# Performance work log

Hardware: AMD Instinct MI355X
Metric: run time of the kernel (lower is better)

## Reference

```python
import jax, jax.numpy as jnp
import numpy as np


def _local_indices(H, W, K):
    # KxK local window per pixel; border neighbors clamped to the image (replicate padding)
    half = K // 2
    d = np.arange(-half, half + 1)
    r = np.clip(np.arange(H)[:, None, None, None] + d[None, None, :, None], 0, H - 1)
    c = np.clip(np.arange(W)[None, :, None, None] + d[None, None, None, :], 0, W - 1)
    return (r * W + c).reshape(H * W, K * K).astype(np.int32)


def setup_inputs():
    B, C, H, W = 2, 32, 128, 128
    K, S = 25, 1024
    N = H * W
    k1, k2, k3, k4 = jax.random.split(jax.random.key(0), 4)
    key_feat = jax.random.normal(k1, (B, C, H, W), dtype=jnp.float32)
    query_feat = jax.random.normal(k2, (B, C, H, W), dtype=jnp.float32)
    segment_target = jax.random.randint(k3, (B, 1, H, W), 0, 64, dtype=jnp.int32)
    local = jnp.broadcast_to(jnp.asarray(_local_indices(H, W, K))[None], (B, N, K * K))
    rand_glob = jax.random.randint(k4, (B, N, S - K * K), 0, N, dtype=jnp.int32)
    sample_inds = jnp.concatenate([local, rand_glob], axis=-1)  # [B, N, S]
    return {"key_feat": key_feat, "query_feat": query_feat,
            "segment_target": segment_target, "sample_inds": sample_inds}


def _affinity_logits(key_f, query_f, sample_inds, chunk=1024):
    # key_f, query_f: [B, N, C]; sample_inds: [B, N, S]
    B, N, C = key_f.shape
    S = sample_inds.shape[-1]
    nchunks = N // chunk
    q_c = query_f.reshape(B, nchunks, chunk, C).transpose(1, 0, 2, 3)
    i_c = sample_inds.reshape(B, nchunks, chunk, S).transpose(1, 0, 2, 3)

    def body(carry, args):
        q, idx = args                                   # [B, chunk, C], [B, chunk, S]
        kg = jax.vmap(lambda kb, ib: kb[ib])(key_f, idx)  # [B, chunk, S, C]
        return carry, jnp.einsum('bnsc,bnc->bns', kg, q)

    _, lc = jax.lax.scan(body, None, (q_c, i_c))        # [nchunks, B, chunk, S]
    logits = lc.transpose(1, 0, 2, 3).reshape(B, N, S)
    return logits * (C ** -0.5)


def _loss(logits, sample_inds, segment_target):
    B, N, S = logits.shape
    seg = segment_target.reshape(B, N)
    samples = jax.vmap(lambda s, i: s[i])(seg, sample_inds)      # [B, N, S]
    targets = (seg[:, :, None] == samples).astype(logits.dtype)
    mask = (seg != 0).astype(logits.dtype)[:, :, None]           # [B, N, 1]
    # weighted_softmax(logits, mask)
    xe = jnp.exp(logits - jnp.max(logits, -1, keepdims=True))
    denom = jnp.sum(xe * mask, -1, keepdims=True)
    y_prob = xe * mask / (denom + 1e-9)
    y_pred = jnp.log(jnp.clip(y_prob, 1e-8, None))
    y_true = targets / (jnp.sum(targets, -1, keepdims=True) + 1e-9)
    # F.kl_div(y_pred, y_true, reduction='none') with 0*log(0) = 0
    kl = jnp.where(y_true > 0,
                   y_true * (jnp.log(jnp.clip(y_true, 1e-30, None)) - y_pred),
                   0.0) * mask
    agg_mask = (jnp.sum(mask, -1) > 0).astype(logits.dtype)
    return jnp.sum(kl) / (jnp.sum(agg_mask) + 1e-9)


def reference(key_feat, query_feat, segment_target, sample_inds):
    B, C, H, W = key_feat.shape
    N = H * W
    key_f = key_feat.reshape(B, C, N).transpose(0, 2, 1)    # [B, N, C]
    query_f = query_feat.reshape(B, C, N).transpose(0, 2, 1)
    logits = _affinity_logits(key_f, query_f, sample_inds)  # [B, N, S], scaled by C**-0.5
    loss = _loss(logits, sample_inds, segment_target)
    return (logits, loss)
```

## Files before the change

### kernel.cpp

```cpp
#include <hip/hip_runtime.h>
#include <stdint.h>

typedef _Float16 h2 __attribute__((ext_vector_type(2)));

static constexpr int CDIM = 32;
static constexpr int NPIX = 16384;
static constexpr int SSAM = 1024;

__device__ __forceinline__ uint16_t f2h(float f) {
    union { _Float16 h; uint16_t u; } c;
    c.h = (_Float16)f;
    return c.u;
}

template<int CTRL>
__device__ __forceinline__ float dpp_add(float x) {
    int y = __builtin_amdgcn_mov_dpp(__float_as_int(x), CTRL, 0xF, 0xF, true);
    return x + __int_as_float(y);
}

__device__ __forceinline__ float dot2(h2 a, h2 b, float c) {
    return __builtin_amdgcn_fdot2(a, b, c, false);
}

__global__ __launch_bounds__(256)
void prep_kernel(const float* __restrict__ key_f,
                 const float* __restrict__ query_f,
                 const int* __restrict__ seg32,
                 uint8_t* __restrict__ key16,
                 uint8_t* __restrict__ q16,
                 uint8_t* __restrict__ seg8,
                 int N, int rows, float scale)
{
    int gI = blockIdx.x * 256 + threadIdx.x;
    if (gI >= rows) return;
    int b = gI / N, n = gI - b * N;
    const size_t cb = (size_t)b * CDIM;

    uint32_t kp[16], qp[16];
#pragma unroll
    for (int c = 0; c < CDIM; c += 2) {
        float k0 = key_f[(cb + c) * N + n];
        float k1 = key_f[(cb + c + 1) * N + n];
        float q0 = query_f[(cb + c) * N + n] * scale;
        float q1 = query_f[(cb + c + 1) * N + n] * scale;
        kp[c >> 1] = (uint32_t)f2h(k0) | ((uint32_t)f2h(k1) << 16);
        qp[c >> 1] = (uint32_t)f2h(q0) | ((uint32_t)f2h(q1) << 16);
    }
    uint4* ko = (uint4*)(key16 + ((size_t)gI << 6));
    uint4* qo = (uint4*)(q16 + ((size_t)gI << 6));
#pragma unroll
    for (int j = 0; j < 4; ++j) {
        ko[j] = make_uint4(kp[4*j], kp[4*j+1], kp[4*j+2], kp[4*j+3]);
        qo[j] = make_uint4(qp[4*j], qp[4*j+1], qp[4*j+2], qp[4*j+3]);
    }
    seg8[gI] = (uint8_t)seg32[gI];
}

__global__ __launch_bounds__(256)
void affinity_coop(const int* __restrict__ inds,
                   const uint8_t* __restrict__ key16,
                   const uint8_t* __restrict__ q16,
                   const uint8_t* __restrict__ seg8,
                   float* __restrict__ out,
                   float* __restrict__ ws_kl)
{
    const int bid  = blockIdx.x;
    const int tid  = threadIdx.x;
    const int b    = bid >> 14;
    const int lane = tid & 63;
    const int w    = tid >> 6;
    const int g    = lane >> 2;
    const int sub  = lane & 3;

    __shared__ __align__(16) int     idx_lds[SSAM];
    __shared__ __align__(16) uint8_t seg_lds[NPIX];
    __shared__ float redA[4], redB[4], redC[4];

    const size_t rowbase = (size_t)bid * SSAM;

    ((int4*)idx_lds)[tid] = ((const int4*)(inds + rowbase))[tid];

    const uint8_t* sbg = seg8 + ((size_t)b << 14);
#pragma unroll
    for (int r = 0; r < 4; ++r)
        ((uint4*)seg_lds)[(r << 8) + tid] = ((const uint4*)sbg)[(r << 8) + tid];

    h2 qh[4];
    {
        union { uint4 u; h2 h[4]; } qc;
        qc.u = *(const uint4*)(q16 + ((size_t)bid << 6) + (sub << 4));
        qh[0] = qc.h[0]; qh[1] = qc.h[1]; qh[2] = qc.h[2]; qh[3] = qc.h[3];
    }
    __syncthreads();

    const int seg_n = (int)seg_lds[bid & 0x3FFF];
    const uint8_t* kb = key16 + ((size_t)b << 20);
    const uint32_t subs = (uint32_t)(sub << 4);
    const int sbase = (w << 8) + g;

    int idxs[16];
#pragma unroll
    for (int i = 0; i < 16; ++i)
        idxs[i] = idx_lds[sbase + (i << 4)];

    uint4 kd[16];
#pragma unroll
    for (int i = 0; i < 16; ++i)
        kd[i] = *(const uint4*)(kb + (((uint32_t)idxs[i] << 6) | subs));

    float lgo[4];
    float m = -1e30f;
#pragma unroll
    for (int i = 0; i < 16; ++i) {
        union { uint4 u; h2 h[4]; } kc; kc.u = kd[i];
        float acc = dot2(kc.h[0], qh[0], 0.f);
        acc = dot2(kc.h[1], qh[1], acc);
        acc = dot2(kc.h[2], qh[2], acc);
        acc = dot2(kc.h[3], qh[3], acc);
        acc = dpp_add<0xB1>(acc);
        acc = dpp_add<0x4E>(acc);
        m = fmaxf(m, acc);
        if (sub == (i & 3)) lgo[i >> 2] = acc;
        if (sub == 0) out[rowbase + sbase + (i << 4)] = acc;
    }

    int tfm = 0;
#pragma unroll
    for (int j = 0; j < 4; ++j) {
        int idx = idx_lds[sbase + ((((j << 2) | sub)) << 4)];
        if ((int)seg_lds[idx] == seg_n) tfm |= 1 << j;
    }

#pragma unroll
    for (int off = 32; off >= 4; off >>= 1)
        m = fmaxf(m, __shfl_xor(m, off, 64));
    if (lane == 0) redA[w] = m;
    __syncthreads();
    m = fmaxf(fmaxf(redA[0], redA[1]), fmaxf(redA[2], redA[3]));

    float e[4];
    float z = 0.f, tcnt = (float)__popc((unsigned)tfm);
#pragma unroll
    for (int j = 0; j < 4; ++j) {
        e[j] = __expf(lgo[j] - m);
        z += e[j];
    }
#pragma unroll
    for (int off = 32; off >= 1; off >>= 1) {
        z    += __shfl_xor(z, off, 64);
        tcnt += __shfl_xor(tcnt, off, 64);
    }
    if (lane == 0) { redB[w] = z; redC[w] = tcnt; }
    __syncthreads();
    const float Z = redB[0] + redB[1] + redB[2] + redB[3];
    const float T = redC[0] + redC[1] + redC[2] + redC[3];

    if (seg_n != 0) {
        float kl = 0.f;
        const float invZ = 1.f / (Z + 1e-9f);
        const float invT = 1.f / (T + 1e-9f);
        const float nlT  = -__logf(T + 1e-9f);
#pragma unroll
        for (int j = 0; j < 4; ++j) {
            if ((tfm >> j) & 1) {
                float p  = e[j] * invZ;
                float yp = __logf(fmaxf(p, 1e-8f));
                kl += invT * (nlT - yp);
            }
        }
#pragma unroll
        for (int off = 32; off >= 1; off >>= 1)
            kl += __shfl_xor(kl, off, 64);
        if (lane == 0) redA[w] = kl;
        __syncthreads();
        if (tid == 0)
            ws_kl[bid] = redA[0] + redA[1] + redA[2] + redA[3];
    } else {
        if (tid == 0) ws_kl[bid] = 0.f;
    }
}

__global__ __launch_bounds__(256)
void affinity_fallback(const float* __restrict__ key_f,
                       const float* __restrict__ query_f,
                       const int*   __restrict__ seg32,
                       const int*   __restrict__ inds,
                       float* __restrict__ out,
                       float* __restrict__ ws_kl,
                       int N, int S, float scale)
{
    const int bid = blockIdx.x;
    const int tid = threadIdx.x;
    const int b   = bid / N;

    __shared__ float q_lds[CDIM];
    __shared__ float redA[4], redB[4], redC[4];

    if (tid < CDIM) {
        int n = bid - b * N;
        q_lds[tid] = query_f[((size_t)(b * CDIM + tid)) * N + n];
    }
    const int seg_n = seg32[bid];
    __syncthreads();

    float q[CDIM];
#pragma unroll
    for (int c = 0; c < CDIM; ++c) q[c] = q_lds[c];

    const size_t rowbase = (size_t)bid * S;
    const int4 iv = ((const int4*)(inds + rowbase))[tid];
    const int idxv[4] = {iv.x, iv.y, iv.z, iv.w};

    float lg[4];
    int   tf[4];
#pragma unroll
    for (int k = 0; k < 4; ++k) {
        int idx = idxv[k];
        tf[k] = (seg32[b * N + idx] == seg_n) ? 1 : 0;
        float acc = 0.f;
#pragma unroll
        for (int c = 0; c < CDIM; ++c)
            acc = fmaf(key_f[((size_t)(b * CDIM + c)) * N + idx], q[c], acc);
        lg[k] = acc * scale;
    }
    ((float4*)(out + rowbase))[tid] = make_float4(lg[0], lg[1], lg[2], lg[3]);

    const int lane = tid & 63, wv = tid >> 6;
    float m = fmaxf(fmaxf(lg[0], lg[1]), fmaxf(lg[2], lg[3]));
#pragma unroll
    for (int off = 32; off >= 1; off >>= 1)
        m = fmaxf(m, __shfl_xor(m, off, 64));
    if (lane == 0) redA[wv] = m;
    __syncthreads();
    m = fmaxf(fmaxf(redA[0], redA[1]), fmaxf(redA[2], redA[3]));

    float e[4], z = 0.f, tcnt = 0.f;
#pragma unroll
    for (int k = 0; k < 4; ++k) {
        e[k] = expf(lg[k] - m);
        z += e[k];
        tcnt += (float)tf[k];
    }
#pragma unroll
    for (int off = 32; off >= 1; off >>= 1) {
        z    += __shfl_xor(z, off, 64);
        tcnt += __shfl_xor(tcnt, off, 64);
    }
    if (lane == 0) { redB[wv] = z; redC[wv] = tcnt; }
    __syncthreads();
    const float Z = redB[0] + redB[1] + redB[2] + redB[3];
    const float T = redC[0] + redC[1] + redC[2] + redC[3];

    float kl = 0.f;
    if (seg_n != 0) {
        const float invZ = 1.f / (Z + 1e-9f);
        const float invT = 1.f / (T + 1e-9f);
        const float nlT  = -logf(T + 1e-9f);
#pragma unroll
        for (int k = 0; k < 4; ++k) {
            if (tf[k]) {
                float p = e[k] * invZ;
                float yp = logf(fmaxf(p, 1e-8f));
                kl += invT * (nlT - yp);
            }
        }
    }
#pragma unroll
    for (int off = 32; off >= 1; off >>= 1)
        kl += __shfl_xor(kl, off, 64);
    if (lane == 0) redA[wv] = kl;
    __syncthreads();
    if (tid == 0)
        ws_kl[bid] = redA[0] + redA[1] + redA[2] + redA[3];
}

__global__ __launch_bounds__(256)
void loss_reduce(const float* __restrict__ ws_kl,
                 const int* __restrict__ seg32,
                 float* __restrict__ out_loss, int rows)
{
    const int tid = threadIdx.x;
    float s = 0.f, c = 0.f;
    for (int i = tid; i < rows; i += 256) {
        s += ws_kl[i];
        c += (seg32[i] != 0) ? 1.f : 0.f;
    }
#pragma unroll
    for (int off = 32; off >= 1; off >>= 1) {
        s += __shfl_xor(s, off, 64);
        c += __shfl_xor(c, off, 64);
    }
    __shared__ float sA[4], sB[4];
    const int lane = tid & 63, wv = tid >> 6;
    if (lane == 0) { sA[wv] = s; sB[wv] = c; }
    __syncthreads();
    if (tid == 0) {
        float ts = sA[0] + sA[1] + sA[2] + sA[3];
        float tc = sB[0] + sB[1] + sB[2] + sB[3];
        out_loss[0] = ts / (tc + 1e-9f);
    }
}

extern "C" void kernel_launch(void* const* d_in, const int* in_sizes, int n_in,
                              void* d_out, int out_size, void* d_ws, size_t ws_size,
                              hipStream_t stream)
{
    const float* key_f   = (const float*)d_in[0];
    const float* query_f = (const float*)d_in[1];
    const int*   seg32   = (const int*)d_in[2];
    const int*   inds    = (const int*)d_in[3];
    float* out = (float*)d_out;

    const int N    = NPIX;
    const int rows = in_sizes[2];
    const int S    = in_sizes[3] / rows;
    const float scale = (float)(1.0 / sqrt((double)CDIM));

    const size_t off_q16 = (size_t)rows * 64;
    const size_t off_s8  = off_q16 + (size_t)rows * 64;
    const size_t off_kl  = (off_s8 + (size_t)rows + 255) & ~(size_t)255;
    const size_t need    = off_kl + (size_t)rows * 4;

    uint8_t* wsb = (uint8_t*)d_ws;
    const bool geom_ok = (S == SSAM) && (rows % N == 0);

    if (ws_size >= need && geom_ok) {
        uint8_t* key16 = wsb;
        uint8_t* q16   = wsb + off_q16;
        uint8_t* seg8  = wsb + off_s8;
        float*   wskl  = (float*)(wsb + off_kl);

        prep_kernel<<<(rows + 255) / 256, 256, 0, stream>>>(
            key_f, query_f, seg32, key16, q16, seg8, N, rows, scale);
        affinity_coop<<<rows, 256, 0, stream>>>(
            inds, key16, q16, seg8, out, wskl);
        loss_reduce<<<1, 256, 0, stream>>>(wskl, seg32, out + (size_t)rows * S, rows);
    } else {
        float* wskl = (float*)d_ws;
        affinity_fallback<<<rows, 256, 0, stream>>>(
            key_f, query_f, seg32, inds, out, wskl, N, S, scale);
        loss_reduce<<<1, 256, 0, stream>>>(wskl, seg32, out + (size_t)rows * S, rows);
    }
}
```

Baseline: 190.2 us.

## Process 16 rows per block with double-buffered index prefetch

The affinity kernel now loops over 16 query rows per block instead of one. The 16KB segment table is loaded into LDS once per block rather than once per row, and the next row's indices and query vector are prefetched into registers while the current row computes. Logit stores are reorganised so each lane writes its four owned values instead of only sub==0 lanes writing all sixteen. The loss reduction now uses 1024 threads. In exchange there are far fewer blocks (2048), which may reduce parallelism for latency hiding, and an extra barrier is added per row.

```diff
diff --git a/kernel.cpp b/kernel.cpp
--- a/kernel.cpp
+++ b/kernel.cpp
@@ -6,6 +6,7 @@
 static constexpr int CDIM = 32;
 static constexpr int NPIX = 16384;
 static constexpr int SSAM = 1024;
+static constexpr int ROWS_PER_BLOCK = 16;
 
 __device__ __forceinline__ uint16_t f2h(float f) {
     union { _Float16 h; uint16_t u; } c;
@@ -58,116 +59,131 @@
 }
 
 __global__ __launch_bounds__(256)
-void affinity_coop(const int* __restrict__ inds,
-                   const uint8_t* __restrict__ key16,
-                   const uint8_t* __restrict__ q16,
-                   const uint8_t* __restrict__ seg8,
-                   float* __restrict__ out,
-                   float* __restrict__ ws_kl)
-{
-    const int bid  = blockIdx.x;
+void affinity_multi(const int* __restrict__ inds,
+                    const uint8_t* __restrict__ key16,
+                    const uint8_t* __restrict__ q16,
+                    const uint8_t* __restrict__ seg8,
+                    float* __restrict__ out,
+                    float* __restrict__ ws_kl)
+{
     const int tid  = threadIdx.x;
-    const int b    = bid >> 14;
+    const int row0 = blockIdx.x * ROWS_PER_BLOCK;
+    const int b    = row0 >> 14;
     const int lane = tid & 63;
     const int w    = tid >> 6;
     const int g    = lane >> 2;
     const int sub  = lane & 3;
 
-    __shared__ __align__(16) int     idx_lds[SSAM];
     __shared__ __align__(16) uint8_t seg_lds[NPIX];
+    __shared__ __align__(16) int     idx_lds[2][SSAM];
     __shared__ float redA[4], redB[4], redC[4];
-
-    const size_t rowbase = (size_t)bid * SSAM;
-
-    ((int4*)idx_lds)[tid] = ((const int4*)(inds + rowbase))[tid];
 
     const uint8_t* sbg = seg8 + ((size_t)b << 14);
 #pragma unroll
     for (int r = 0; r < 4; ++r)
         ((uint4*)seg_lds)[(r << 8) + tid] = ((const uint4*)sbg)[(r << 8) + tid];
-
-    h2 qh[4];
-    {
-        union { uint4 u; h2 h[4]; } qc;
-        qc.u = *(const uint4*)(q16 + ((size_t)bid << 6) + (sub << 4));
-        qh[0] = qc.h[0]; qh[1] = qc.h[1]; qh[2] = qc.h[2]; qh[3] = qc.h[3];
-    }
-    __syncthreads();
-
-    const int seg_n = (int)seg_lds[bid & 0x3FFF];
+    ((int4*)idx_lds[0])[tid] = ((const int4*)(inds + ((size_t)row0 << 10)))[tid];
+    uint4 qcur = *(const uint4*)(q16 + ((size_t)row0 << 6) + (sub << 4));
+    __syncthreads();
+
     const uint8_t* kb = key16 + ((size_t)b << 20);
     const uint32_t subs = (uint32_t)(sub << 4);
     const int sbase = (w << 8) + g;
 
-    int idxs[16];
-#pragma unroll
-    for (int i = 0; i < 16; ++i)
-        idxs[i] = idx_lds[sbase + (i << 4)];
-
-    uint4 kd[16];
-#pragma unroll
-    for (int i = 0; i < 16; ++i)
-        kd[i] = *(const uint4*)(kb + (((uint32_t)idxs[i] << 6) | subs));
-
-    float lgo[4];
-    float m = -1e30f;
-#pragma unroll
-    for (int i = 0; i < 16; ++i) {
-        union { uint4 u; h2 h[4]; } kc; kc.u = kd[i];
-        float acc = dot2(kc.h[0], qh[0], 0.f);
-        acc = dot2(kc.h[1], qh[1], acc);
-        acc = dot2(kc.h[2], qh[2], acc);
-        acc = dot2(kc.h[3], qh[3], acc);
-        acc = dpp_add<0xB1>(acc);
-        acc = dpp_add<0x4E>(acc);
-        m = fmaxf(m, acc);
-        if (sub == (i & 3)) lgo[i >> 2] = acc;
-        if (sub == 0) out[rowbase + sbase + (i << 4)] = acc;
-    }
-
-    int tfm = 0;
-#pragma unroll
-    for (int j = 0; j < 4; ++j) {
-        int idx = idx_lds[sbase + ((((j << 2) | sub)) << 4)];
-        if ((int)seg_lds[idx] == seg_n) tfm |= 1 << j;
-    }
-
-#pragma unroll
-    for (int off = 32; off >= 4; off >>= 1)
-        m = fmaxf(m, __shfl_xor(m, off, 64));
-    if (lane == 0) redA[w] = m;
-    __syncthreads();
-    m = fmaxf(fmaxf(redA[0], redA[1]), fmaxf(redA[2], redA[3]));
-
-    float e[4];
-    float z = 0.f, tcnt = (float)__popc((unsigned)tfm);
-#pragma unroll
-    for (int j = 0; j < 4; ++j) {
-        e[j] = __expf(lgo[j] - m);
-        z += e[j];
-    }
-#pragma unroll
-    for (int off = 32; off >= 1; off >>= 1) {
-        z    += __shfl_xor(z, off, 64);
-        tcnt += __shfl_xor(tcnt, off, 64);
-    }
-    if (lane == 0) { redB[w] = z; redC[w] = tcnt; }
-    __syncthreads();
-    const float Z = redB[0] + redB[1] + redB[2] + redB[3];
-    const float T = redC[0] + redC[1] + redC[2] + redC[3];
-
-    if (seg_n != 0) {
+    for (int r = 0; r < ROWS_PER_BLOCK; ++r) {
+        const int row = row0 + r;
+        const int* cur = idx_lds[r & 1];
+        const bool hasNext = (r + 1 < ROWS_PER_BLOCK);
+
+        h2 qh0, qh1, qh2, qh3;
+        {
+            union { uint4 u; h2 h[4]; } qc; qc.u = qcur;
+            qh0 = qc.h[0]; qh1 = qc.h[1]; qh2 = qc.h[2]; qh3 = qc.h[3];
+        }
+        const int seg_n = (int)seg_lds[row & 0x3FFF];
+
+        int idxs[16];
+#pragma unroll
+        for (int i = 0; i < 16; ++i)
+            idxs[i] = cur[sbase + (i << 4)];
+
+        uint4 kd[16];
+#pragma unroll
+        for (int i = 0; i < 16; ++i)
+            kd[i] = *(const uint4*)(kb + (((uint32_t)idxs[i] << 6) | subs));
+        __builtin_amdgcn_sched_barrier(0);
+
+        int4 pre; uint4 qnext;
+        if (hasNext) {
+            pre   = ((const int4*)(inds + ((size_t)(row + 1) << 10)))[tid];
+            qnext = *(const uint4*)(q16 + ((size_t)(row + 1) << 6) + (sub << 4));
+        }
+        __builtin_amdgcn_sched_barrier(0);
+
+        int tfm = 0;
+#pragma unroll
+        for (int j = 0; j < 4; ++j) {
+            int idx = cur[sbase + (((j << 2) | sub) << 4)];
+            if ((int)seg_lds[idx] == seg_n) tfm |= 1 << j;
+        }
+
+        float lgo0 = 0.f, lgo1 = 0.f, lgo2 = 0.f, lgo3 = 0.f;
+        float m = -1e30f;
+#pragma unroll
+        for (int i = 0; i < 16; ++i) {
+            union { uint4 u; h2 h[4]; } kc; kc.u = kd[i];
+            float acc = dot2(kc.h[0], qh0, 0.f);
+            acc = dot2(kc.h[1], qh1, acc);
+            acc = dot2(kc.h[2], qh2, acc);
+            acc = dot2(kc.h[3], qh3, acc);
+            acc = dpp_add<0xB1>(acc);
+            acc = dpp_add<0x4E>(acc);
+            m = fmaxf(m, acc);
+            if (sub == (i & 3)) {
+                if ((i >> 2) == 0) lgo0 = acc;
+                if ((i >> 2) == 1) lgo1 = acc;
+                if ((i >> 2) == 2) lgo2 = acc;
+                if ((i >> 2) == 3) lgo3 = acc;
+            }
+        }
+
+        const size_t rowbase = (size_t)row << 10;
+        float* op = out + rowbase + (w << 8) + (sub << 4) + g;
+        op[0]   = lgo0;
+        op[64]  = lgo1;
+        op[128] = lgo2;
+        op[192] = lgo3;
+
+#pragma unroll
+        for (int off = 32; off >= 4; off >>= 1)
+            m = fmaxf(m, __shfl_xor(m, off, 64));
+        if (lane == 0) redA[w] = m;
+        __syncthreads();
+        m = fmaxf(fmaxf(redA[0], redA[1]), fmaxf(redA[2], redA[3]));
+
+        float e0 = __expf(lgo0 - m), e1 = __expf(lgo1 - m);
+        float e2 = __expf(lgo2 - m), e3 = __expf(lgo3 - m);
+        float z = (e0 + e1) + (e2 + e3);
+        float tcnt = (float)__popc((unsigned)tfm);
+#pragma unroll
+        for (int off = 32; off >= 1; off >>= 1) {
+            z    += __shfl_xor(z, off, 64);
+            tcnt += __shfl_xor(tcnt, off, 64);
+        }
+        if (lane == 0) { redB[w] = z; redC[w] = tcnt; }
+        __syncthreads();
+        const float Z = redB[0] + redB[1] + redB[2] + redB[3];
+        const float T = redC[0] + redC[1] + redC[2] + redC[3];
+
         float kl = 0.f;
-        const float invZ = 1.f / (Z + 1e-9f);
-        const float invT = 1.f / (T + 1e-9f);
-        const float nlT  = -__logf(T + 1e-9f);
-#pragma unroll
-        for (int j = 0; j < 4; ++j) {
-            if ((tfm >> j) & 1) {
-                float p  = e[j] * invZ;
-                float yp = __logf(fmaxf(p, 1e-8f));
-                kl += invT * (nlT - yp);
-            }
+        if (seg_n != 0) {
+            const float invZ = 1.f / (Z + 1e-9f);
+            const float invT = 1.f / (T + 1e-9f);
+            const float nlT  = -__logf(T + 1e-9f);
+            if (tfm & 1) kl += invT * (nlT - __logf(fmaxf(e0 * invZ, 1e-8f)));
+            if (tfm & 2) kl += invT * (nlT - __logf(fmaxf(e1 * invZ, 1e-8f)));
+            if (tfm & 4) kl += invT * (nlT - __logf(fmaxf(e2 * invZ, 1e-8f)));
+            if (tfm & 8) kl += invT * (nlT - __logf(fmaxf(e3 * invZ, 1e-8f)));
         }
 #pragma unroll
         for (int off = 32; off >= 1; off >>= 1)
@@ -175,9 +191,13 @@
         if (lane == 0) redA[w] = kl;
         __syncthreads();
         if (tid == 0)
-            ws_kl[bid] = redA[0] + redA[1] + redA[2] + redA[3];
-    } else {
-        if (tid == 0) ws_kl[bid] = 0.f;
+            ws_kl[row] = redA[0] + redA[1] + redA[2] + redA[3];
+
+        if (hasNext) {
+            ((int4*)idx_lds[(r + 1) & 1])[tid] = pre;
+            qcur = qnext;
+        }
+        __syncthreads();
     }
 }
 
@@ -275,14 +295,14 @@
         ws_kl[bid] = redA[0] + redA[1] + redA[2] + redA[3];
 }
 
-__global__ __launch_bounds__(256)
+__global__ __launch_bounds__(1024)
 void loss_reduce(const float* __restrict__ ws_kl,
                  const int* __restrict__ seg32,
                  float* __restrict__ out_loss, int rows)
 {
     const int tid = threadIdx.x;
     float s = 0.f, c = 0.f;
-    for (int i = tid; i < rows; i += 256) {
+    for (int i = tid; i < rows; i += 1024) {
         s += ws_kl[i];
         c += (seg32[i] != 0) ? 1.f : 0.f;
     }
@@ -291,13 +311,14 @@
         s += __shfl_xor(s, off, 64);
         c += __shfl_xor(c, off, 64);
     }
-    __shared__ float sA[4], sB[4];
+    __shared__ float sA[16], sB[16];
     const int lane = tid & 63, wv = tid >> 6;
     if (lane == 0) { sA[wv] = s; sB[wv] = c; }
     __syncthreads();
     if (tid == 0) {
-        float ts = sA[0] + sA[1] + sA[2] + sA[3];
-        float tc = sB[0] + sB[1] + sB[2] + sB[3];
+        float ts = 0.f, tc = 0.f;
+#pragma unroll
+        for (int k = 0; k < 16; ++k) { ts += sA[k]; tc += sB[k]; }
         out_loss[0] = ts / (tc + 1e-9f);
     }
 }
@@ -323,7 +344,8 @@
     const size_t need    = off_kl + (size_t)rows * 4;
 
     uint8_t* wsb = (uint8_t*)d_ws;
-    const bool geom_ok = (S == SSAM) && (rows % N == 0);
+    const bool geom_ok = (S == SSAM) && (rows % N == 0) &&
+                         (rows % ROWS_PER_BLOCK == 0);
 
     if (ws_size >= need && geom_ok) {
         uint8_t* key16 = wsb;
@@ -333,13 +355,13 @@
 
         prep_kernel<<<(rows + 255) / 256, 256, 0, stream>>>(
             key_f, query_f, seg32, key16, q16, seg8, N, rows, scale);
-        affinity_coop<<<rows, 256, 0, stream>>>(
+        affinity_multi<<<rows / ROWS_PER_BLOCK, 256, 0, stream>>>(
             inds, key16, q16, seg8, out, wskl);
-        loss_reduce<<<1, 256, 0, stream>>>(wskl, seg32, out + (size_t)rows * S, rows);
+        loss_reduce<<<1, 1024, 0, stream>>>(wskl, seg32, out + (size_t)rows * S, rows);
     } else {
         float* wskl = (float*)d_ws;
         affinity_fallback<<<rows, 256, 0, stream>>>(
             key_f, query_f, seg32, inds, out, wskl, N, S, scale);
-        loss_reduce<<<1, 256, 0, stream>>>(wskl, seg32, out + (size_t)rows * S, rows);
-    }
-}
+        loss_reduce<<<1, 1024, 0, stream>>>(wskl, seg32, out + (size_t)rows * S, rows);
+    }
+}
```

Result: faster. 168.7 us (-11.3%).
